# Optimization experiments

Measured on AMD Instinct MI355X. Metric: run time of the kernel, lower is better.

The kernel has to match this reference:

```python
import jax, jax.numpy as jnp
import numpy as np

B, T, C, S, H, K = 32, 128, 32, 256, 64, 3  # T == 2*H required by final Linear(hidden*2, 1)


def setup_inputs() -> dict:
    key = jax.random.key(0)
    k1, k2, k3, k4 = jax.random.split(key, 4)
    x = jax.random.normal(k1, (B, T, C, S), jnp.float32)
    # ConvLSTMCell: Conv1d(C+H -> 4H, kernel K, padding same), gate order i,f,o,g
    Wc = jax.random.normal(k2, (4 * H, C + H, K), jnp.float32) * 0.05
    bc = jnp.zeros((4 * H,), jnp.float32)
    # final Linear(hidden*2 = T, 1)
    Wl = jax.random.normal(k3, (1, T), jnp.float32) * 0.05
    bl = jnp.zeros((1,), jnp.float32)
    return {"x": x, "Wc": Wc, "bc": bc, "Wl": Wl, "bl": bl}


def _cell(x_t, h, c, Wc, bc):
    # x_t: (B, C, T); h, c: (B, H, T). Conv over the T axis, 'same' padding.
    z = jnp.concatenate([x_t, h], axis=1)  # (B, C+H, T)
    conv = jax.lax.conv_general_dilated(
        z, Wc, window_strides=(1,), padding='SAME',
        dimension_numbers=('NCH', 'OIH', 'NCH')) + bc[None, :, None]
    ci, cf, co, cg = jnp.split(conv, 4, axis=1)
    i = jax.nn.sigmoid(ci)
    f = jax.nn.sigmoid(cf)
    o = jax.nn.sigmoid(co)
    g = jnp.tanh(cg)
    c_next = f * c + i * g
    h_next = o * jnp.tanh(c_next)
    return h_next, c_next


def reference(x, Wc, bc, Wl, bl):
    # x: (B, T, C, S); sequential scan over spatial axis S with (h, c) recurrence.
    xs = jnp.transpose(x, (3, 0, 2, 1))  # (S, B, C, T)
    h0 = jnp.zeros((x.shape[0], H, x.shape[1]), x.dtype)

    def step(carry, xt):
        h, c = carry
        h2, c2 = _cell(xt, h, c, Wc, bc)
        return (h2, c2), h2

    _, hs = jax.lax.scan(step, (h0, h0), xs)  # hs: (S, B, H, T)
    lstm_out = jnp.transpose(hs, (1, 0, 2, 3))  # (B, S, H, T)
    out = jax.nn.sigmoid(jnp.einsum('bsht,ot->bso', lstm_out, Wl)[..., None].squeeze(-1)[..., None] * 0 + jnp.einsum('bsht,ot->bsho', lstm_out, Wl) + bl)
    return out  # (B, S, H, 1)
```

## Files before the change

kernel.cpp:

```cpp
#include <hip/hip_runtime.h>


#define Bb 32
#define Tt 128
#define Cc 32
#define Ss 256
#define Hh 64
#define ZST 104

typedef __bf16 bf16x8 __attribute__((ext_vector_type(8)));
typedef short  short8 __attribute__((ext_vector_type(8)));
typedef float  f32x4  __attribute__((ext_vector_type(4)));
typedef unsigned short u16;
typedef unsigned int   u32;

__device__ __forceinline__ u16 f2bf(float f) {
    u32 u = __float_as_uint(f);
    u = (u + 0x7FFFu + ((u >> 16) & 1u)) >> 16;
    return (u16)u;
}
__device__ __forceinline__ float fsig(float x) {
    float e = __expf(-x);
    return __builtin_amdgcn_rcpf(1.0f + e);
}
__device__ __forceinline__ float ftanh_(float x) {
    float e = __expf(2.0f * x);
    return 1.0f - 2.0f * __builtin_amdgcn_rcpf(e + 1.0f);
}

__global__ __launch_bounds__(256) void xpose_kernel(const float* __restrict__ x,
                                                    u16* __restrict__ xT) {
    __shared__ u16 tile[64][130];
    const int tc0 = blockIdx.x * 128;
    const int s0  = blockIdx.y * 64;
    const int b   = blockIdx.z;
    const int tid = threadIdx.x;
    const float* xb = x + (size_t)b * (Tt * Cc * Ss);
#pragma unroll
    for (int i = 0; i < 32; ++i) {
        const int tcr = (tid >> 6) + 4 * i;
        const int sr  = tid & 63;
        tile[sr][tcr] = f2bf(xb[(size_t)(tc0 + tcr) * Ss + s0 + sr]);
    }
    __syncthreads();
    u32* xTo = (u32*)(xT + (size_t)b * (Ss * Tt * Cc));
#pragma unroll
    for (int j = 0; j < 16; ++j) {
        const int sw = (tid >> 6) + 4 * j;
        const int tw = (tid & 63) * 2;
        xTo[(((size_t)(s0 + sw)) * (Tt * Cc) + tc0 + tw) >> 1] = *(const u32*)&tile[sw][tw];
    }
}

__global__ __launch_bounds__(512) void convlstm8_kernel(
    const float* __restrict__ Wc, const float* __restrict__ bc,
    const float* __restrict__ Wl, const float* __restrict__ bl,
    const u16* __restrict__ xT, float* __restrict__ out, int zkeep) {

    __shared__ u16  zbuf[2][130][ZST];
    __shared__ float red[8][16];
    __shared__ u16  zpad[14000];

    const int b    = blockIdx.x;
    const int tid  = threadIdx.x;
    const int w    = tid >> 6;
    const int lane = tid & 63;
    const int l15  = lane & 15;
    const int q    = lane >> 4;
    const int ht   = w >> 1;
    const int th   = w & 1;

    if (zkeep) {
        zpad[tid] = (u16)tid;
        out[tid & 63] += (float)zpad[(tid * 7) & 13999];
    }

    {
        u32* z32 = (u32*)&zbuf[0][0][0];
        for (int i = tid; i < (2 * 130 * ZST) / 2; i += 512) z32[i] = 0;
    }

    bf16x8 afr[4][3][3];
#pragma unroll
    for (int g = 0; g < 4; ++g)
#pragma unroll
        for (int k = 0; k < 3; ++k)
#pragma unroll
            for (int ks = 0; ks < 3; ++ks) {
                const int gc = 64 * g + 16 * ht + l15;
                short8 t;
#pragma unroll
                for (int j = 0; j < 8; ++j)
                    t[j] = (short)f2bf(Wc[gc * 288 + (32 * ks + 8 * q + j) * 3 + k]);
                afr[g][k][ks] = __builtin_bit_cast(bf16x8, t);
            }

    f32x4 bcv[4];
#pragma unroll
    for (int g = 0; g < 4; ++g) bcv[g] = *(const f32x4*)&bc[64 * g + 16 * ht + 4 * q];
    float wlv[4];
#pragma unroll
    for (int nj = 0; nj < 4; ++nj) wlv[nj] = Wl[64 * th + 16 * nj + l15];
    const float bl0 = bl[0];

    float cst[16];
#pragma unroll
    for (int i = 0; i < 16; ++i) cst[i] = 0.0f;

    const int xt = tid >> 2;
    const int xc = (tid & 3) * 8;
    const u16* xTb = xT + (size_t)b * (Ss * Tt * Cc);

    {
        uint4 xv0 = *(const uint4*)(xTb + xt * 32 + xc);
        __syncthreads();
        *(uint4*)&zbuf[0][1 + xt][xc] = xv0;
        __syncthreads();
    }

    float* outb = out + (size_t)b * (Ss * Hh);
    int p = 0;

    for (int s = 0; s < Ss; ++s) {
        uint4 xv;
        const bool havex = (s + 1) < Ss;
        if (havex) xv = *(const uint4*)(xTb + (size_t)(s + 1) * (Tt * Cc) + xt * 32 + xc);

        if (tid < 64 && s > 0) {
            float v = red[(tid >> 4) * 2][tid & 15] + red[(tid >> 4) * 2 + 1][tid & 15] + bl0;
            outb[(size_t)(s - 1) * Hh + tid] = fsig(v);
        }
        __syncthreads();

        const u16 (*zb)[ZST] = zbuf[p];
        u16 (*zn)[ZST] = zbuf[p ^ 1];

        float partial[4] = {0.f, 0.f, 0.f, 0.f};

#pragma unroll
        for (int half = 0; half < 2; ++half) {
            f32x4 acc[4][2];
#pragma unroll
            for (int g = 0; g < 4; ++g) {
                acc[g][0] = bcv[g];
                acc[g][1] = bcv[g];
            }
#pragma unroll
            for (int njl = 0; njl < 2; ++njl) {
                const int nj = half * 2 + njl;
                const int tb = 64 * th + 16 * nj + l15;
#pragma unroll
                for (int k = 0; k < 3; ++k)
#pragma unroll
                    for (int ks = 0; ks < 3; ++ks) {
                        bf16x8 bfr = *(const bf16x8*)&zb[tb + k][32 * ks + 8 * q];
                        acc[0][njl] = __builtin_amdgcn_mfma_f32_16x16x32_bf16(afr[0][k][ks], bfr, acc[0][njl], 0, 0, 0);
                        acc[1][njl] = __builtin_amdgcn_mfma_f32_16x16x32_bf16(afr[1][k][ks], bfr, acc[1][njl], 0, 0, 0);
                        acc[2][njl] = __builtin_amdgcn_mfma_f32_16x16x32_bf16(afr[2][k][ks], bfr, acc[2][njl], 0, 0, 0);
                        acc[3][njl] = __builtin_amdgcn_mfma_f32_16x16x32_bf16(afr[3][k][ks], bfr, acc[3][njl], 0, 0, 0);
                    }
            }

#pragma unroll
            for (int njl = 0; njl < 2; ++njl) {
                const int nj = half * 2 + njl;
                u16 hp[4];
#pragma unroll
                for (int r = 0; r < 4; ++r) {
                    const float ig = fsig(acc[0][njl][r]);
                    const float fg = fsig(acc[1][njl][r]);
                    const float og = fsig(acc[2][njl][r]);
                    const float gg = ftanh_(acc[3][njl][r]);
                    const float cv = fg * cst[nj * 4 + r] + ig * gg;
                    cst[nj * 4 + r] = cv;
                    const float hv = og * ftanh_(cv);
                    partial[r] += hv * wlv[nj];
                    hp[r] = f2bf(hv);
                }
                uint2 hw;
                hw.x = (u32)hp[0] | ((u32)hp[1] << 16);
                hw.y = (u32)hp[2] | ((u32)hp[3] << 16);
                *(uint2*)&zn[1 + 64 * th + 16 * nj + l15][32 + 16 * ht + 4 * q] = hw;
            }
        }

        if (havex) *(uint4*)&zn[1 + xt][xc] = xv;

#pragma unroll
        for (int r = 0; r < 4; ++r) {
#pragma unroll
            for (int offl = 1; offl <= 8; offl <<= 1)
                partial[r] += __shfl_xor(partial[r], offl, 64);
        }
        if (l15 == 0) {
#pragma unroll
            for (int r = 0; r < 4; ++r) red[w][4 * q + r] = partial[r];
        }
        __syncthreads();
        p ^= 1;
    }

    if (tid < 64) {
        float v = red[(tid >> 4) * 2][tid & 15] + red[(tid >> 4) * 2 + 1][tid & 15] + bl0;
        outb[(size_t)(Ss - 1) * Hh + tid] = fsig(v);
    }
}

extern "C" void kernel_launch(void* const* d_in, const int* in_sizes, int n_in,
                              void* d_out, int out_size, void* d_ws, size_t ws_size,
                              hipStream_t stream) {
    const float* x  = (const float*)d_in[0];
    const float* Wc = (const float*)d_in[1];
    const float* bc = (const float*)d_in[2];
    const float* Wl = (const float*)d_in[3];
    const float* bl = (const float*)d_in[4];
    float* out = (float*)d_out;
    u16*   xT  = (u16*)d_ws;

    dim3 tgrid(Tt * Cc / 128, Ss / 64, Bb);
    xpose_kernel<<<tgrid, 256, 0, stream>>>(x, xT);
    convlstm8_kernel<<<Bb, 512, 0, stream>>>(Wc, bc, Wl, bl, xT, out, 0);
}
```

Before: 1.409 ms.

## Stagger half order across wave groups and raise MFMA priority

Waves 4-7 now process the two column halves in reverse order from waves 0-3, so their MFMA phases and transcendental gate phases interleave on the SIMDs. MFMA sections are wrapped in s_setprio to favour matrix issue. The bias is moved from register-initialised accumulators into LDS and added in the gate math, which frees VGPRs. The launch bounds now ask for 2 blocks per CU, and the unused zpad padding array is removed. With only 32 blocks the occupancy hint probably matters less than the lower register pressure, and the extra LDS bias reads add a little ALU and LDS traffic.

```diff
diff --git a/kernel.cpp b/kernel.cpp
--- a/kernel.cpp
+++ b/kernel.cpp
@@ -52,14 +52,14 @@
     }
 }
 
-__global__ __launch_bounds__(512) void convlstm8_kernel(
+__global__ __launch_bounds__(512, 2) void convlstm9_kernel(
     const float* __restrict__ Wc, const float* __restrict__ bc,
     const float* __restrict__ Wl, const float* __restrict__ bl,
-    const u16* __restrict__ xT, float* __restrict__ out, int zkeep) {
+    const u16* __restrict__ xT, float* __restrict__ out) {
 
     __shared__ u16  zbuf[2][130][ZST];
     __shared__ float red[8][16];
-    __shared__ u16  zpad[14000];
+    __shared__ float bcl[256];
 
     const int b    = blockIdx.x;
     const int tid  = threadIdx.x;
@@ -69,16 +69,13 @@
     const int q    = lane >> 4;
     const int ht   = w >> 1;
     const int th   = w & 1;
-
-    if (zkeep) {
-        zpad[tid] = (u16)tid;
-        out[tid & 63] += (float)zpad[(tid * 7) & 13999];
-    }
+    const int grp  = w >> 2;
 
     {
         u32* z32 = (u32*)&zbuf[0][0][0];
         for (int i = tid; i < (2 * 130 * ZST) / 2; i += 512) z32[i] = 0;
     }
+    if (tid < 256) bcl[tid] = bc[tid];
 
     bf16x8 afr[4][3][3];
 #pragma unroll
@@ -95,9 +92,6 @@
                 afr[g][k][ks] = __builtin_bit_cast(bf16x8, t);
             }
 
-    f32x4 bcv[4];
-#pragma unroll
-    for (int g = 0; g < 4; ++g) bcv[g] = *(const f32x4*)&bc[64 * g + 16 * ht + 4 * q];
     float wlv[4];
 #pragma unroll
     for (int nj = 0; nj < 4; ++nj) wlv[nj] = Wl[64 * th + 16 * nj + l15];
@@ -138,13 +132,17 @@
         float partial[4] = {0.f, 0.f, 0.f, 0.f};
 
 #pragma unroll
-        for (int half = 0; half < 2; ++half) {
+        for (int hh = 0; hh < 2; ++hh) {
+            const int half = hh ^ grp;
+
             f32x4 acc[4][2];
 #pragma unroll
             for (int g = 0; g < 4; ++g) {
-                acc[g][0] = bcv[g];
-                acc[g][1] = bcv[g];
-            }
+                acc[g][0] = (f32x4){0.f, 0.f, 0.f, 0.f};
+                acc[g][1] = (f32x4){0.f, 0.f, 0.f, 0.f};
+            }
+
+            __builtin_amdgcn_s_setprio(1);
 #pragma unroll
             for (int njl = 0; njl < 2; ++njl) {
                 const int nj = half * 2 + njl;
@@ -160,6 +158,7 @@
                         acc[3][njl] = __builtin_amdgcn_mfma_f32_16x16x32_bf16(afr[3][k][ks], bfr, acc[3][njl], 0, 0, 0);
                     }
             }
+            __builtin_amdgcn_s_setprio(0);
 
 #pragma unroll
             for (int njl = 0; njl < 2; ++njl) {
@@ -167,10 +166,11 @@
                 u16 hp[4];
 #pragma unroll
                 for (int r = 0; r < 4; ++r) {
-                    const float ig = fsig(acc[0][njl][r]);
-                    const float fg = fsig(acc[1][njl][r]);
-                    const float og = fsig(acc[2][njl][r]);
-                    const float gg = ftanh_(acc[3][njl][r]);
+                    const int hl = 4 * q + r;
+                    const float ig = fsig(acc[0][njl][r] + bcl[0   + 16 * ht + hl]);
+                    const float fg = fsig(acc[1][njl][r] + bcl[64  + 16 * ht + hl]);
+                    const float og = fsig(acc[2][njl][r] + bcl[128 + 16 * ht + hl]);
+                    const float gg = ftanh_(acc[3][njl][r] + bcl[192 + 16 * ht + hl]);
                     const float cv = fg * cst[nj * 4 + r] + ig * gg;
                     cst[nj * 4 + r] = cv;
                     const float hv = og * ftanh_(cv);
@@ -219,5 +219,5 @@
 
     dim3 tgrid(Tt * Cc / 128, Ss / 64, Bb);
     xpose_kernel<<<tgrid, 256, 0, stream>>>(x, xT);
-    convlstm8_kernel<<<Bb, 512, 0, stream>>>(Wc, bc, Wl, bl, xT, out, 0);
-}
+    convlstm9_kernel<<<Bb, 512, 0, stream>>>(Wc, bc, Wl, bl, xT, out);
+}
```

Result: faster. 1.327 ms (-5.8%).
